# Kernel optimization log

Hardware: AMD Instinct MI355X
Metric: run time of the kernel (lower is better)

The kernel has to match this reference:

```python
import jax, jax.numpy as jnp
import numpy as np

B, D, N, K, T = 8192, 256, 2048, 512, 8
M_MARGIN = 1.0
LAMBDA_ORTHO = 1e-3
EPS = 1e-10


def _l2(a, b):
    # squared L2 distance along last axis
    return jnp.sum((a - b) ** 2, axis=-1)


def setup_inputs() -> dict:
    key = jax.random.key(0)
    k1, k2, k3, k4, k5 = jax.random.split(key, 5)
    return {
        "v": jax.random.normal(k1, (B, D), dtype=jnp.float32),
        "vhat": jax.random.normal(k2, (B, D), dtype=jnp.float32),
        "g": jax.random.uniform(k3, (B, K), dtype=jnp.float32),
        "F": jax.random.normal(k4, (K, D), dtype=jnp.float32),
        "negatives": jax.random.normal(k5, (N, D), dtype=jnp.float32),
        "mask": jnp.ones((B,), dtype=bool),
    }


def reference(v, vhat, g, F, negatives, mask):
    maskf = mask.astype(v.dtype)
    msum = maskf.sum()

    # ---- contrastive loss (vectorized over the N-negatives loop) ----
    true_dist = _l2(vhat, v)                                   # [B]
    neg_dist = _l2(vhat[:, None, :], negatives[None, :, :])    # [B, N]
    per = jnp.maximum(1.0 + true_dist[:, None] - neg_dist, 0.0)
    ju_per = per.mean(axis=1) * maskf                          # [B]
    Ju = jnp.where(msum == 0, 0.0, ju_per.sum() / msum)

    # ---- focal triplet loss (topk smallest g, gather F rows) ----
    _, idx = jax.lax.top_k(-g, T)                              # [B, T] indices of t smallest
    g_tz = jnp.take_along_axis(g, idx, axis=1)                 # [B, T]
    F_t = F[idx]                                               # [B, T, D]
    g_t = g_tz / (g_tz.sum(axis=1, keepdims=True) + EPS)
    m_t = M_MARGIN * (1.0 - g_t) ** 2                          # [B, T]
    d_neg = _l2(vhat[:, None, :], F_t)                         # [B, T]
    cur = jnp.maximum(m_t + true_dist[:, None] - d_neg, 0.0)
    jt_per = cur.sum(axis=1) * maskf
    Jt = jnp.where(msum == 0, 0.0, jt_per.sum() / msum)

    # ---- orthogonality regularizer: ||F F^T - I||_F, then squared ----
    gram = F @ F.T - jnp.eye(K, dtype=F.dtype)
    ortho = jnp.sqrt(jnp.sum(gram ** 2))

    Jz = Ju + Jt + LAMBDA_ORTHO * ortho ** 2
    return Jz
```

## Files before the change

kernel.cpp:

```cpp
#include <hip/hip_runtime.h>

#define B_N 8192
#define D_N 256
#define N_N 2048
#define K_N 512
#define T_N 8

using short8  = __attribute__((ext_vector_type(8))) short;
using floatx4 = __attribute__((ext_vector_type(4))) float;


__device__ __forceinline__ float wave_reduce_sum(float x) {
  #pragma unroll
  for (int off = 32; off > 0; off >>= 1) x += __shfl_down(x, off, 64);
  return x;
}

__device__ __forceinline__ unsigned int f2bf(float x) {
  unsigned u = __float_as_uint(x);
  return (u + 0x7fffu + ((u >> 16) & 1u)) >> 16;
}

__device__ __forceinline__ unsigned int pack2bf(float x, float y) {
  return f2bf(x) | (f2bf(y) << 16);
}

__device__ __forceinline__ void gload16(const unsigned short* g, unsigned short* l) {
  __builtin_amdgcn_global_load_lds(
      (const __attribute__((address_space(1))) unsigned int*)g,
      (__attribute__((address_space(3))) unsigned int*)l, 16, 0, 0);
}

#define CSWAP(a, b)                                              \
  {                                                              \
    bool sw_ = sv[a] > sv[b];                                    \
    float tv_ = sw_ ? sv[a] : sv[b];                             \
    sv[a] = sw_ ? sv[b] : sv[a];                                 \
    sv[b] = tv_;                                                 \
    int ti_ = sw_ ? si[a] : si[b];                               \
    si[a] = sw_ ? si[b] : si[a];                                 \
    si[b] = ti_;                                                 \
  }

__global__ __launch_bounds__(256) void prep_kernel(
    const float* __restrict__ v, const float* __restrict__ vhat,
    const float* __restrict__ neg, const float* __restrict__ F,
    const float* __restrict__ g, const int* __restrict__ mask,
    unsigned short* __restrict__ vhat_bf, unsigned short* __restrict__ neg_bf,
    unsigned short* __restrict__ F_bf,
    float* __restrict__ cb, float* __restrict__ nn2, float* __restrict__ fn2,
    float* __restrict__ selc, int* __restrict__ seli,
    float* __restrict__ msum_part) {
  int lane = threadIdx.x & 63;
  int wave = threadIdx.x >> 6;
  int row = (blockIdx.x << 2) + wave;
  if (blockIdx.x < 32) {
    float m = (mask[blockIdx.x * 256 + threadIdx.x] != 0) ? 1.0f : 0.0f;
    m = wave_reduce_sum(m);
    __shared__ float mred[4];
    if (lane == 0) mred[wave] = m;
    __syncthreads();
    if (threadIdx.x == 0)
      msum_part[blockIdx.x] = mred[0] + mred[1] + mred[2] + mred[3];
  }
  if (row < B_N) {
    const float4 a = *(const float4*)(vhat + (size_t)row * D_N + lane * 4);
    const float4 b = *(const float4*)(v + (size_t)row * D_N + lane * 4);
    float dx = a.x - b.x, dy = a.y - b.y, dz = a.z - b.z, dw = a.w - b.w;
    float t = dx * dx + dy * dy + dz * dz + dw * dw;
    float n = a.x * a.x + a.y * a.y + a.z * a.z + a.w * a.w;
    uint2 p;
    p.x = pack2bf(a.x, a.y);
    p.y = pack2bf(a.z, a.w);
    *(uint2*)(vhat_bf + (size_t)row * D_N + lane * 4) = p;
    t = wave_reduce_sum(t);
    n = wave_reduce_sum(n);
    if (lane == 0) cb[row] = 1.0f + t - n;
    const float* grow = g + (size_t)row * K_N;
    float sv[8];
    int si[8];
    {
      float4 g0 = *(const float4*)(grow + lane * 8);
      float4 g1 = *(const float4*)(grow + lane * 8 + 4);
      sv[0] = g0.x; sv[1] = g0.y; sv[2] = g0.z; sv[3] = g0.w;
      sv[4] = g1.x; sv[5] = g1.y; sv[6] = g1.z; sv[7] = g1.w;
      #pragma unroll
      for (int j = 0; j < 8; ++j) si[j] = lane * 8 + j;
    }
    CSWAP(0,1) CSWAP(2,3) CSWAP(4,5) CSWAP(6,7)
    CSWAP(0,2) CSWAP(1,3) CSWAP(4,6) CSWAP(5,7)
    CSWAP(1,2) CSWAP(5,6)
    CSWAP(0,4) CSWAP(1,5) CSWAP(2,6) CSWAP(3,7)
    CSWAP(2,4) CSWAP(3,5)
    CSWAP(1,2) CSWAP(3,4) CSWAP(5,6)
    #pragma unroll
    for (int rr = 0; rr < 6; ++rr) {
      const int msk = 1 << rr;
      float pv[8];
      int pi[8];
      #pragma unroll
      for (int j = 0; j < 8; ++j) {
        pv[j] = __shfl_xor(sv[j], msk, 64);
        pi[j] = __shfl_xor(si[j], msk, 64);
      }
      float cv[8];
      int ci[8];
      #pragma unroll
      for (int j = 0; j < 8; ++j) {
        bool mine = sv[j] <= pv[7 - j];
        cv[j] = mine ? sv[j] : pv[7 - j];
        ci[j] = mine ? si[j] : pi[7 - j];
      }
      #pragma unroll
      for (int j = 0; j < 8; ++j) { sv[j] = cv[j]; si[j] = ci[j]; }
      CSWAP(0,4) CSWAP(1,5) CSWAP(2,6) CSWAP(3,7)
      CSWAP(0,2) CSWAP(1,3) CSWAP(4,6) CSWAP(5,7)
      CSWAP(0,1) CSWAP(2,3) CSWAP(4,5) CSWAP(6,7)
    }
    float gsum = 1e-10f;
    #pragma unroll
    for (int t8 = 0; t8 < T_N; ++t8) gsum += sv[t8];
    if (lane == 0) {
      float base = t - n;
      #pragma unroll
      for (int t8 = 0; t8 < T_N; ++t8) {
        float gt = sv[t8] / gsum;
        float mt = (1.0f - gt) * (1.0f - gt);
        selc[(size_t)row * T_N + t8] = mt + base;
        seli[(size_t)row * T_N + t8] = si[t8];
      }
    }
  } else if (row < B_N + N_N) {
    int r = row - B_N;
    const float4 a = *(const float4*)(neg + (size_t)r * D_N + lane * 4);
    float n = a.x * a.x + a.y * a.y + a.z * a.z + a.w * a.w;
    uint2 p;
    p.x = pack2bf(a.x, a.y);
    p.y = pack2bf(a.z, a.w);
    *(uint2*)(neg_bf + (size_t)r * D_N + lane * 4) = p;
    n = wave_reduce_sum(n);
    if (lane == 0) nn2[r] = n;
  } else {
    int r = row - (B_N + N_N);
    const float4 a = *(const float4*)(F + (size_t)r * D_N + lane * 4);
    float n = a.x * a.x + a.y * a.y + a.z * a.z + a.w * a.w;
    uint2 p;
    p.x = pack2bf(a.x, a.y);
    p.y = pack2bf(a.z, a.w);
    *(uint2*)(F_bf + (size_t)r * D_N + lane * 4) = p;
    n = wave_reduce_sum(n);
    if (lane == 0) fn2[r] = n;
  }
}

__global__ __launch_bounds__(256) void main_kernel(
    const unsigned short* __restrict__ vhat_bf, const unsigned short* __restrict__ neg_bf,
    const unsigned short* __restrict__ F_bf,
    const float* __restrict__ cb, const float* __restrict__ nn2,
    const float* __restrict__ fn2, const int* __restrict__ mask,
    const float* __restrict__ selc, const int* __restrict__ seli,
    float* __restrict__ ju_part, float* __restrict__ or_part,
    float* __restrict__ jt_part) {
  __shared__ __align__(16) unsigned char smem[16384];
  const int bx = blockIdx.x;
  const int tid = threadIdx.x;
  const int lane = tid & 63;
  const int wave = tid >> 6;

  unsigned short* AsU = (unsigned short*)smem;
  unsigned short* BsU = AsU + 4096;
  int r0, c0;
  const unsigned short *Abase, *Bbase;
  int seg;
  if (bx < 1024) {
    seg = 0;
    r0 = (bx >> 4) * 128;
    c0 = (bx & 15) * 128;
    Abase = vhat_bf;
    Bbase = neg_bf;
  } else if (bx < 1040) {
    seg = 1;
    int o = bx - 1024;
    r0 = (o >> 2) * 128;
    c0 = (o & 3) * 128;
    Abase = F_bf;
    Bbase = F_bf;
  } else {
    seg = 2;
    int o = bx - 1040;
    r0 = (o >> 2) * 128;
    c0 = (o & 3) * 128;
    Abase = vhat_bf;
    Bbase = F_bf;
  }
  const int wx = wave & 1, wy = wave >> 1;

  const int c_slot = lane & 3;
  const int rA0 = wave * 32 + (lane >> 2);
  const int rA1 = rA0 + 16;
  const int cg0 = c_slot ^ ((rA0 >> 1) & 3);
  const int cg1 = c_slot ^ ((rA1 >> 1) & 3);
  const unsigned short* gA0 = Abase + (size_t)(r0 + rA0) * D_N + cg0 * 8;
  const unsigned short* gA1 = Abase + (size_t)(r0 + rA1) * D_N + cg1 * 8;
  const unsigned short* gB0 = Bbase + (size_t)(c0 + rA0) * D_N + cg0 * 8;
  const unsigned short* gB1 = Bbase + (size_t)(c0 + rA1) * D_N + cg1 * 8;
  unsigned short* lA0 = AsU + wave * 1024 + lane * 8;
  unsigned short* lA1 = lA0 + 512;
  unsigned short* lB0 = BsU + wave * 1024 + lane * 8;
  unsigned short* lB1 = lB0 + 512;

  const int fr = lane & 15;
  const int fc = lane >> 4;
  int aoff[4], boff[4];
  #pragma unroll
  for (int i = 0; i < 4; ++i) {
    int ra = wy * 64 + i * 16 + fr;
    aoff[i] = ra * 32 + (fc ^ ((ra >> 1) & 3)) * 8;
    int rb = wx * 64 + i * 16 + fr;
    boff[i] = rb * 32 + (fc ^ ((rb >> 1) & 3)) * 8;
  }

  floatx4 acc[4][4];
  #pragma unroll
  for (int i = 0; i < 4; ++i)
    #pragma unroll
    for (int j = 0; j < 4; ++j)
      acc[i][j] = floatx4{0.0f, 0.0f, 0.0f, 0.0f};

  for (int k0 = 0; k0 < D_N; k0 += 32) {
    __syncthreads();
    gload16(gA0 + k0, lA0);
    gload16(gA1 + k0, lA1);
    gload16(gB0 + k0, lB0);
    gload16(gB1 + k0, lB1);
    __syncthreads();
    short8 af[4], bf[4];
    #pragma unroll
    for (int i = 0; i < 4; ++i) af[i] = *(const short8*)(AsU + aoff[i]);
    #pragma unroll
    for (int j = 0; j < 4; ++j) bf[j] = *(const short8*)(BsU + boff[j]);
    #pragma unroll
    for (int i = 0; i < 4; ++i)
      #pragma unroll
      for (int j = 0; j < 4; ++j)
        acc[i][j] = __builtin_amdgcn_mfma_f32_16x16x32_bf16(af[i], bf[j], acc[i][j], 0, 0, 0);
  }

  float* red = (float*)smem;
  if (seg == 0) {
    float nns[4];
    #pragma unroll
    for (int j = 0; j < 4; ++j)
      nns[j] = nn2[c0 + wx * 64 + j * 16 + (lane & 15)];
    float lsum = 0.0f;
    #pragma unroll
    for (int i = 0; i < 4; ++i) {
      #pragma unroll
      for (int r = 0; r < 4; ++r) {
        int b = r0 + wy * 64 + i * 16 + (lane >> 4) * 4 + r;
        float cbb = cb[b];
        float mf = (mask[b] != 0) ? 1.0f : 0.0f;
        float rs = 0.0f;
        #pragma unroll
        for (int j = 0; j < 4; ++j) {
          float val = cbb + 2.0f * acc[i][j][r] - nns[j];
          rs += fmaxf(val, 0.0f);
        }
        lsum += mf * rs;
      }
    }
    lsum = wave_reduce_sum(lsum);
    __syncthreads();
    if (lane == 0) red[wave] = lsum;
    __syncthreads();
    if (tid == 0) ju_part[bx] = red[0] + red[1] + red[2] + red[3];
  } else if (seg == 1) {
    float lsum = 0.0f;
    #pragma unroll
    for (int i = 0; i < 4; ++i) {
      #pragma unroll
      for (int r = 0; r < 4; ++r) {
        int gi = r0 + wy * 64 + i * 16 + (lane >> 4) * 4 + r;
        #pragma unroll
        for (int j = 0; j < 4; ++j) {
          int gj = c0 + wx * 64 + j * 16 + (lane & 15);
          float s = (gi == gj) ? (fn2[gi] - 1.0f) : acc[i][j][r];
          lsum += s * s;
        }
      }
    }
    lsum = wave_reduce_sum(lsum);
    __syncthreads();
    if (lane == 0) red[wave] = lsum;
    __syncthreads();
    if (tid == 0) or_part[bx - 1024] = red[0] + red[1] + red[2] + red[3];
  } else {
    float* Wt = (float*)smem;
    const int quad = lane >> 4, col15 = lane & 15;
    const int rl = tid >> 3;
    const int t8 = tid & 7;
    float jts = 0.0f;
    #pragma unroll
    for (int i = 0; i < 4; ++i) {
      __syncthreads();
      #pragma unroll
      for (int r = 0; r < 4; ++r) {
        int row_local = wy * 16 + quad * 4 + r;
        #pragma unroll
        for (int j = 0; j < 4; ++j)
          Wt[row_local * 128 + wx * 64 + j * 16 + col15] = acc[i][j][r];
      }
      __syncthreads();
      int b = r0 + (rl & 15) + i * 16 + (rl >> 4) * 64;
      int idx = seli[(size_t)b * 8 + t8];
      int c = idx - c0;
      if ((unsigned)c < 128u) {
        float w = Wt[rl * 128 + c];
        float term = selc[(size_t)b * 8 + t8] + 2.0f * w - fn2[idx];
        float mf = (mask[b] != 0) ? 1.0f : 0.0f;
        jts += mf * fmaxf(term, 0.0f);
      }
    }
    jts = wave_reduce_sum(jts);
    __syncthreads();
    if (lane == 0) red[wave] = jts;
    __syncthreads();
    if (tid == 0) jt_part[bx - 1040] = red[0] + red[1] + red[2] + red[3];
  }
}

__global__ __launch_bounds__(256) void finalize_kernel(
    const float* __restrict__ jt_part, const float* __restrict__ ju_part,
    const float* __restrict__ or_part, const float* __restrict__ msum_part,
    float* __restrict__ out) {
  int tid = threadIdx.x;
  float sjt = 0.0f, sju = 0.0f, sor = 0.0f, sm = 0.0f;
  for (int i = tid; i < 1024; i += 256) sju += ju_part[i];
  if (tid < 256) sjt = jt_part[tid];
  if (tid < 16) sor = or_part[tid];
  if (tid < 32) sm = msum_part[tid];
  sjt = wave_reduce_sum(sjt);
  sju = wave_reduce_sum(sju);
  sor = wave_reduce_sum(sor);
  sm  = wave_reduce_sum(sm);
  __shared__ float red[4][4];
  int lane = tid & 63, w = tid >> 6;
  if (lane == 0) {
    red[w][0] = sjt; red[w][1] = sju; red[w][2] = sor; red[w][3] = sm;
  }
  __syncthreads();
  if (tid == 0) {
    float jt = red[0][0] + red[1][0] + red[2][0] + red[3][0];
    float ju = red[0][1] + red[1][1] + red[2][1] + red[3][1];
    float oo = red[0][2] + red[1][2] + red[2][2] + red[3][2];
    float ms = red[0][3] + red[1][3] + red[2][3] + red[3][3];
    float Ju = (ms == 0.0f) ? 0.0f : ju / ((float)N_N * ms);
    float Jt = (ms == 0.0f) ? 0.0f : jt / ms;
    out[0] = Ju + Jt + 1.0e-3f * oo;
  }
}

extern "C" void kernel_launch(void* const* d_in, const int* in_sizes, int n_in,
                              void* d_out, int out_size, void* d_ws, size_t ws_size,
                              hipStream_t stream) {
  (void)in_sizes; (void)n_in; (void)out_size; (void)ws_size;
  const float* v    = (const float*)d_in[0];
  const float* vhat = (const float*)d_in[1];
  const float* g    = (const float*)d_in[2];
  const float* F    = (const float*)d_in[3];
  const float* neg  = (const float*)d_in[4];
  const int*   mask = (const int*)d_in[5];

  float* ws = (float*)d_ws;
  float* cb        = ws;
  float* nn2       = ws + 8192;
  float* fn2       = ws + 10240;
  float* ju_part   = ws + 10752;
  float* jt_part   = ws + 11776;
  float* or_part   = ws + 12032;
  float* msum_part = ws + 12048;
  float* selc      = ws + 12080;
  int*   seli      = (int*)(ws + 77616);
  unsigned short* vhat_bf = (unsigned short*)(ws + 143152);
  unsigned short* neg_bf  = vhat_bf + (size_t)B_N * D_N;
  unsigned short* F_bf    = neg_bf + (size_t)N_N * D_N;

  prep_kernel<<<(B_N + N_N + K_N) / 4, 256, 0, stream>>>(
      v, vhat, neg, F, g, mask, vhat_bf, neg_bf, F_bf, cb, nn2, fn2,
      selc, seli, msum_part);
  main_kernel<<<1024 + 16 + 256, 256, 0, stream>>>(
      vhat_bf, neg_bf, F_bf, cb, nn2, fn2, mask, selc, seli,
      ju_part, or_part, jt_part);
  finalize_kernel<<<1, 256, 0, stream>>>(jt_part, ju_part, or_part, msum_part,
                                         (float*)d_out);
}
```

Before: 116.3 us.

## Compute triplet loss in prep via F row gathers, fuse finalize, exploit Gram symmetry

The focal triplet term is now computed in fp32 directly in the prep kernel by gathering the 8 selected F rows per sample. This replaces 256 vhat x F GEMM tiles and their shared-memory scatter. The Gram regularizer uses only upper-triangular tiles weighted by two, cutting those tiles from 16 to 10. The separate finalize kernel is removed in favour of atomic accumulation plus a last-block reduction. The cost is extra global reads of F rows in prep and atomic contention, and the atomic float sums make the result order-dependent.

```diff
diff --git a/kernel.cpp b/kernel.cpp
--- a/kernel.cpp
+++ b/kernel.cpp
@@ -12,7 +12,7 @@
 
 __device__ __forceinline__ float wave_reduce_sum(float x) {
   #pragma unroll
-  for (int off = 32; off > 0; off >>= 1) x += __shfl_down(x, off, 64);
+  for (int off = 32; off > 0; off >>= 1) x += __shfl_xor(x, off, 64);
   return x;
 }
 
@@ -49,15 +49,19 @@
     unsigned short* __restrict__ vhat_bf, unsigned short* __restrict__ neg_bf,
     unsigned short* __restrict__ F_bf,
     float* __restrict__ cb, float* __restrict__ nn2, float* __restrict__ fn2,
-    float* __restrict__ selc, int* __restrict__ seli,
-    float* __restrict__ msum_part) {
+    float* __restrict__ jt_part, float* __restrict__ msum_part,
+    float* __restrict__ acc, int* __restrict__ cnt) {
   int lane = threadIdx.x & 63;
   int wave = threadIdx.x >> 6;
   int row = (blockIdx.x << 2) + wave;
+  __shared__ float mred[4];
+  __shared__ float jred[4];
+  if (blockIdx.x == 0 && threadIdx.x == 0) {
+    acc[0] = 0.0f; acc[1] = 0.0f; *cnt = 0;
+  }
   if (blockIdx.x < 32) {
     float m = (mask[blockIdx.x * 256 + threadIdx.x] != 0) ? 1.0f : 0.0f;
     m = wave_reduce_sum(m);
-    __shared__ float mred[4];
     if (lane == 0) mred[wave] = m;
     __syncthreads();
     if (threadIdx.x == 0)
@@ -117,19 +121,33 @@
       CSWAP(0,2) CSWAP(1,3) CSWAP(4,6) CSWAP(5,7)
       CSWAP(0,1) CSWAP(2,3) CSWAP(4,5) CSWAP(6,7)
     }
+    float4 fr8[8];
+    #pragma unroll
+    for (int t8 = 0; t8 < T_N; ++t8) {
+      int idx = __builtin_amdgcn_readfirstlane(si[t8]);
+      fr8[t8] = *(const float4*)(F + (size_t)idx * D_N + lane * 4);
+    }
     float gsum = 1e-10f;
     #pragma unroll
     for (int t8 = 0; t8 < T_N; ++t8) gsum += sv[t8];
-    if (lane == 0) {
-      float base = t - n;
-      #pragma unroll
-      for (int t8 = 0; t8 < T_N; ++t8) {
-        float gt = sv[t8] / gsum;
-        float mt = (1.0f - gt) * (1.0f - gt);
-        selc[(size_t)row * T_N + t8] = mt + base;
-        seli[(size_t)row * T_N + t8] = si[t8];
-      }
-    }
+    float base = t - n;
+    float jts = 0.0f;
+    #pragma unroll
+    for (int t8 = 0; t8 < T_N; ++t8) {
+      float4 f = fr8[t8];
+      float s = 2.0f * (a.x * f.x + a.y * f.y + a.z * f.z + a.w * f.w)
+              - (f.x * f.x + f.y * f.y + f.z * f.z + f.w * f.w);
+      s = wave_reduce_sum(s);
+      float gt = sv[t8] / gsum;
+      float mt = 1.0f - gt;
+      mt *= mt;
+      jts += fmaxf(mt + base + s, 0.0f);
+    }
+    float mf = (mask[row] != 0) ? 1.0f : 0.0f;
+    if (lane == 0) jred[wave] = jts * mf;
+    __syncthreads();
+    if (threadIdx.x == 0)
+      jt_part[blockIdx.x] = jred[0] + jred[1] + jred[2] + jred[3];
   } else if (row < B_N + N_N) {
     int r = row - B_N;
     const float4 a = *(const float4*)(neg + (size_t)r * D_N + lane * 4);
@@ -158,10 +176,10 @@
     const unsigned short* __restrict__ F_bf,
     const float* __restrict__ cb, const float* __restrict__ nn2,
     const float* __restrict__ fn2, const int* __restrict__ mask,
-    const float* __restrict__ selc, const int* __restrict__ seli,
-    float* __restrict__ ju_part, float* __restrict__ or_part,
-    float* __restrict__ jt_part) {
+    const float* __restrict__ jt_part, const float* __restrict__ msum_part,
+    float* __restrict__ acc, int* __restrict__ cnt, float* __restrict__ out) {
   __shared__ __align__(16) unsigned char smem[16384];
+  __shared__ int lastFlag;
   const int bx = blockIdx.x;
   const int tid = threadIdx.x;
   const int lane = tid & 63;
@@ -172,26 +190,24 @@
   int r0, c0;
   const unsigned short *Abase, *Bbase;
   int seg;
-  if (bx < 1024) {
-    seg = 0;
-    r0 = (bx >> 4) * 128;
-    c0 = (bx & 15) * 128;
-    Abase = vhat_bf;
-    Bbase = neg_bf;
-  } else if (bx < 1040) {
+  float wgt = 1.0f;
+  if (bx < 10) {
     seg = 1;
-    int o = bx - 1024;
-    r0 = (o >> 2) * 128;
-    c0 = (o & 3) * 128;
+    int o = bx;
+    int ti = (o < 4) ? 0 : (o < 7) ? 1 : (o < 9) ? 2 : 3;
+    int tj = (o < 4) ? o : (o < 7) ? o - 3 : (o < 9) ? o - 5 : 3;
+    r0 = ti * 128;
+    c0 = tj * 128;
+    wgt = (ti == tj) ? 1.0f : 2.0f;
     Abase = F_bf;
     Bbase = F_bf;
   } else {
-    seg = 2;
-    int o = bx - 1040;
-    r0 = (o >> 2) * 128;
-    c0 = (o & 3) * 128;
+    seg = 0;
+    int o = bx - 10;
+    r0 = (o >> 4) * 128;
+    c0 = (o & 15) * 128;
     Abase = vhat_bf;
-    Bbase = F_bf;
+    Bbase = neg_bf;
   }
   const int wx = wave & 1, wy = wave >> 1;
 
@@ -220,12 +236,12 @@
     boff[i] = rb * 32 + (fc ^ ((rb >> 1) & 3)) * 8;
   }
 
-  floatx4 acc[4][4];
+  floatx4 acc4[4][4];
   #pragma unroll
   for (int i = 0; i < 4; ++i)
     #pragma unroll
     for (int j = 0; j < 4; ++j)
-      acc[i][j] = floatx4{0.0f, 0.0f, 0.0f, 0.0f};
+      acc4[i][j] = floatx4{0.0f, 0.0f, 0.0f, 0.0f};
 
   for (int k0 = 0; k0 < D_N; k0 += 32) {
     __syncthreads();
@@ -243,16 +259,15 @@
     for (int i = 0; i < 4; ++i)
       #pragma unroll
       for (int j = 0; j < 4; ++j)
-        acc[i][j] = __builtin_amdgcn_mfma_f32_16x16x32_bf16(af[i], bf[j], acc[i][j], 0, 0, 0);
-  }
-
-  float* red = (float*)smem;
+        acc4[i][j] = __builtin_amdgcn_mfma_f32_16x16x32_bf16(af[i], bf[j], acc4[i][j], 0, 0, 0);
+  }
+
+  float lsum = 0.0f;
   if (seg == 0) {
     float nns[4];
     #pragma unroll
     for (int j = 0; j < 4; ++j)
       nns[j] = nn2[c0 + wx * 64 + j * 16 + (lane & 15)];
-    float lsum = 0.0f;
     #pragma unroll
     for (int i = 0; i < 4; ++i) {
       #pragma unroll
@@ -263,19 +278,13 @@
         float rs = 0.0f;
         #pragma unroll
         for (int j = 0; j < 4; ++j) {
-          float val = cbb + 2.0f * acc[i][j][r] - nns[j];
+          float val = cbb + 2.0f * acc4[i][j][r] - nns[j];
           rs += fmaxf(val, 0.0f);
         }
         lsum += mf * rs;
       }
     }
-    lsum = wave_reduce_sum(lsum);
-    __syncthreads();
-    if (lane == 0) red[wave] = lsum;
-    __syncthreads();
-    if (tid == 0) ju_part[bx] = red[0] + red[1] + red[2] + red[3];
-  } else if (seg == 1) {
-    float lsum = 0.0f;
+  } else {
     #pragma unroll
     for (int i = 0; i < 4; ++i) {
       #pragma unroll
@@ -284,79 +293,45 @@
         #pragma unroll
         for (int j = 0; j < 4; ++j) {
           int gj = c0 + wx * 64 + j * 16 + (lane & 15);
-          float s = (gi == gj) ? (fn2[gi] - 1.0f) : acc[i][j][r];
+          float s = (gi == gj) ? (fn2[gi] - 1.0f) : acc4[i][j][r];
           lsum += s * s;
         }
       }
     }
-    lsum = wave_reduce_sum(lsum);
-    __syncthreads();
-    if (lane == 0) red[wave] = lsum;
-    __syncthreads();
-    if (tid == 0) or_part[bx - 1024] = red[0] + red[1] + red[2] + red[3];
-  } else {
-    float* Wt = (float*)smem;
-    const int quad = lane >> 4, col15 = lane & 15;
-    const int rl = tid >> 3;
-    const int t8 = tid & 7;
-    float jts = 0.0f;
-    #pragma unroll
-    for (int i = 0; i < 4; ++i) {
-      __syncthreads();
-      #pragma unroll
-      for (int r = 0; r < 4; ++r) {
-        int row_local = wy * 16 + quad * 4 + r;
-        #pragma unroll
-        for (int j = 0; j < 4; ++j)
-          Wt[row_local * 128 + wx * 64 + j * 16 + col15] = acc[i][j][r];
-      }
-      __syncthreads();
-      int b = r0 + (rl & 15) + i * 16 + (rl >> 4) * 64;
-      int idx = seli[(size_t)b * 8 + t8];
-      int c = idx - c0;
-      if ((unsigned)c < 128u) {
-        float w = Wt[rl * 128 + c];
-        float term = selc[(size_t)b * 8 + t8] + 2.0f * w - fn2[idx];
-        float mf = (mask[b] != 0) ? 1.0f : 0.0f;
-        jts += mf * fmaxf(term, 0.0f);
-      }
-    }
-    jts = wave_reduce_sum(jts);
-    __syncthreads();
-    if (lane == 0) red[wave] = jts;
-    __syncthreads();
-    if (tid == 0) jt_part[bx - 1040] = red[0] + red[1] + red[2] + red[3];
-  }
-}
-
-__global__ __launch_bounds__(256) void finalize_kernel(
-    const float* __restrict__ jt_part, const float* __restrict__ ju_part,
-    const float* __restrict__ or_part, const float* __restrict__ msum_part,
-    float* __restrict__ out) {
-  int tid = threadIdx.x;
-  float sjt = 0.0f, sju = 0.0f, sor = 0.0f, sm = 0.0f;
-  for (int i = tid; i < 1024; i += 256) sju += ju_part[i];
-  if (tid < 256) sjt = jt_part[tid];
-  if (tid < 16) sor = or_part[tid];
-  if (tid < 32) sm = msum_part[tid];
-  sjt = wave_reduce_sum(sjt);
-  sju = wave_reduce_sum(sju);
-  sor = wave_reduce_sum(sor);
-  sm  = wave_reduce_sum(sm);
-  __shared__ float red[4][4];
-  int lane = tid & 63, w = tid >> 6;
-  if (lane == 0) {
-    red[w][0] = sjt; red[w][1] = sju; red[w][2] = sor; red[w][3] = sm;
-  }
+    lsum *= wgt;
+  }
+
+  lsum = wave_reduce_sum(lsum);
+  float* red = (float*)smem;
+  __syncthreads();
+  if (lane == 0) red[wave] = lsum;
   __syncthreads();
   if (tid == 0) {
-    float jt = red[0][0] + red[1][0] + red[2][0] + red[3][0];
-    float ju = red[0][1] + red[1][1] + red[2][1] + red[3][1];
-    float oo = red[0][2] + red[1][2] + red[2][2] + red[3][2];
-    float ms = red[0][3] + red[1][3] + red[2][3] + red[3][3];
-    float Ju = (ms == 0.0f) ? 0.0f : ju / ((float)N_N * ms);
-    float Jt = (ms == 0.0f) ? 0.0f : jt / ms;
-    out[0] = Ju + Jt + 1.0e-3f * oo;
+    float partial = red[0] + red[1] + red[2] + red[3];
+    atomicAdd(&acc[seg == 0 ? 0 : 1], partial);
+    __threadfence();
+    lastFlag = (atomicAdd(cnt, 1) == (int)gridDim.x - 1) ? 1 : 0;
+  }
+  __syncthreads();
+  if (lastFlag) {
+    __threadfence();
+    float sjt = 0.0f, sm = 0.0f;
+    for (int i = tid; i < 2048; i += 256) sjt += jt_part[i];
+    if (tid < 32) sm = msum_part[tid];
+    sjt = wave_reduce_sum(sjt);
+    sm = wave_reduce_sum(sm);
+    __syncthreads();
+    if (lane == 0) { red[wave] = sjt; red[4 + wave] = sm; }
+    __syncthreads();
+    if (tid == 0) {
+      float jt = red[0] + red[1] + red[2] + red[3];
+      float ms = red[4] + red[5] + red[6] + red[7];
+      float ju = atomicAdd(&acc[0], 0.0f);
+      float oo = atomicAdd(&acc[1], 0.0f);
+      float Ju = (ms == 0.0f) ? 0.0f : ju / ((float)N_N * ms);
+      float Jt = (ms == 0.0f) ? 0.0f : jt / ms;
+      out[0] = Ju + Jt + 1.0e-3f * oo;
+    }
   }
 }
 
@@ -375,22 +350,18 @@
   float* cb        = ws;
   float* nn2       = ws + 8192;
   float* fn2       = ws + 10240;
-  float* ju_part   = ws + 10752;
-  float* jt_part   = ws + 11776;
-  float* or_part   = ws + 12032;
-  float* msum_part = ws + 12048;
-  float* selc      = ws + 12080;
-  int*   seli      = (int*)(ws + 77616);
-  unsigned short* vhat_bf = (unsigned short*)(ws + 143152);
+  float* jt_part   = ws + 10752;
+  float* msum_part = ws + 12800;
+  float* acc       = ws + 12832;
+  int*   cnt       = (int*)(ws + 12834);
+  unsigned short* vhat_bf = (unsigned short*)(ws + 12848);
   unsigned short* neg_bf  = vhat_bf + (size_t)B_N * D_N;
   unsigned short* F_bf    = neg_bf + (size_t)N_N * D_N;
 
   prep_kernel<<<(B_N + N_N + K_N) / 4, 256, 0, stream>>>(
       v, vhat, neg, F, g, mask, vhat_bf, neg_bf, F_bf, cb, nn2, fn2,
-      selc, seli, msum_part);
-  main_kernel<<<1024 + 16 + 256, 256, 0, stream>>>(
-      vhat_bf, neg_bf, F_bf, cb, nn2, fn2, mask, selc, seli,
-      ju_part, or_part, jt_part);
-  finalize_kernel<<<1, 256, 0, stream>>>(jt_part, ju_part, or_part, msum_part,
-                                         (float*)d_out);
-}
+      jt_part, msum_part, acc, cnt);
+  main_kernel<<<10 + 1024, 256, 0, stream>>>(
+      vhat_bf, neg_bf, F_bf, cb, nn2, fn2, mask, jt_part, msum_part,
+      acc, cnt, (float*)d_out);
+}
```

New measurement: 138.1 us. +18.8%, slower.
